# Performance work log

Measured on AMD Instinct MI355X. Metric: run time of the kernel, lower is better.

Reference implementation:

```python
import jax, jax.numpy as jnp
import numpy as np

B, S, D, H = 2, 2048, 1024, 16
HD = D // H  # 64


def setup_inputs() -> dict:
    key = jax.random.key(0)
    k1, k2, k3, k4, k5, k6 = jax.random.split(key, 6)
    x = jax.random.normal(k1, (B, S, D), dtype=jnp.float32)
    # binary mask source (1.0 = masked-out position), multiplied by -1e9 inside
    mask = (jax.random.uniform(k2, (B, S, S), dtype=jnp.float32) < 0.1).astype(jnp.float32)
    lim = 1.0 / np.sqrt(D)
    Wqkv = jax.random.uniform(k3, (D, 3 * D), dtype=jnp.float32, minval=-lim, maxval=lim)
    bqkv = jax.random.uniform(k4, (3 * D,), dtype=jnp.float32, minval=-lim, maxval=lim)
    Wo = jax.random.uniform(k5, (D, D), dtype=jnp.float32, minval=-lim, maxval=lim)
    bo = jax.random.uniform(k6, (D,), dtype=jnp.float32, minval=-lim, maxval=lim)
    return {"x": x, "mask": mask, "Wqkv": Wqkv, "bqkv": bqkv, "Wo": Wo, "bo": bo}


def reference(x, mask, Wqkv, bqkv, Wo, bo):
    b, s, d = x.shape
    qkv = x @ Wqkv + bqkv                              # [B,S,3D]
    qkv = qkv.reshape(b, s, 3, H, HD).transpose(2, 0, 3, 1, 4)  # [3,B,H,S,HD]
    q, k, v = qkv[0], qkv[1], qkv[2]
    scale = 1.0 / jnp.sqrt(jnp.float32(HD))
    scores = jnp.einsum('bhqd,bhkd->bhqk', q, k) * scale
    scores = scores + mask[:, None, :, :] * (-1e9)     # broadcast over heads
    attn = jax.nn.softmax(scores, axis=-1)             # [B,H,S,S]
    values = jnp.einsum('bhqk,bhkd->bhqd', attn, v)    # [B,H,S,HD]
    # faithful to source: permute(1,0,2,3) then reshape(B,S,H*HD)
    values = values.transpose(1, 0, 2, 3).reshape(b, s, H * HD)
    return values @ Wo + bo
```

## Files before the change

### kernel.cpp

```cpp
#include <hip/hip_runtime.h>
#include <stdint.h>

#define BB 2
#define SS 2048
#define DD 1024
#define HH 16
#define HD 64
#define BH 32
#define BS 4096

typedef short bf16x8 __attribute__((ext_vector_type(8)));
typedef float f32x4 __attribute__((ext_vector_type(4)));

static __device__ __forceinline__ unsigned short f2bf(float f) {
    union { float f; unsigned int u; } x;
    x.f = f;
    unsigned int u = x.u;
    unsigned int r = u + 0x7FFFu + ((u >> 16) & 1u);
    return (unsigned short)(r >> 16);
}

static __device__ __forceinline__ void gld16(unsigned short* lds, const unsigned short* g) {
    __builtin_amdgcn_global_load_lds(
        (const __attribute__((address_space(1))) unsigned int*)g,
        (__attribute__((address_space(3))) unsigned int*)lds,
        16, 0, 0);
}

__global__ __launch_bounds__(256) void prep(
    const float* __restrict__ x, unsigned short* __restrict__ xb,
    const float* __restrict__ Wqkv, unsigned short* __restrict__ WqkvT,
    const float* __restrict__ Wo, unsigned short* __restrict__ WoT,
    const float* __restrict__ mask, unsigned int* __restrict__ mbitsT,
    unsigned int* __restrict__ kmaxsq) {
    __shared__ float tile[32][33];
    int bid = blockIdx.x;
    int tid = threadIdx.x;
    if (bid < 4096) {
        int i = (bid * 256 + tid) * 4;
        float4 v = *(const float4*)(x + i);
        ushort4 o;
        o.x = f2bf(v.x); o.y = f2bf(v.y); o.z = f2bf(v.z); o.w = f2bf(v.w);
        *(ushort4*)(xb + i) = o;
    } else if (bid < 8192) {
        const float* W;
        unsigned short* WT;
        int N, t;
        if (bid < 7168) { W = Wqkv; WT = WqkvT; N = 3072; t = bid - 4096; }
        else            { W = Wo;   WT = WoT;   N = 1024; t = bid - 7168; }
        const int K = 1024;
        int nx = N >> 5;
        int n0 = (t % nx) * 32, k0 = (t / nx) * 32;
        int tx = tid & 31, ty = tid >> 5;
#pragma unroll
        for (int i = 0; i < 4; i++)
            tile[ty + i * 8][tx] = W[(size_t)(k0 + ty + i * 8) * N + n0 + tx];
        __syncthreads();
#pragma unroll
        for (int i = 0; i < 4; i++)
            WT[(size_t)(n0 + ty + i * 8) * K + k0 + tx] = f2bf(tile[tx][ty + i * 8]);
    } else if (bid == 8192) {
        if (tid < BH) kmaxsq[tid] = 0u;
    } else {
        size_t i = (size_t)(bid - 8193) * 256 + tid;
        float v = mask[i];
        unsigned long long bal = __ballot(v != 0.0f);
        int lane = tid & 63;
        int kw = (int)((i & 2047) >> 5);
        int sq = (int)((i >> 11) & 2047);
        int b = (int)(i >> 22);
        if (lane == 0)
            mbitsT[((size_t)b * 64 + kw) * 2048 + sq] = (unsigned int)bal;
        else if (lane == 32)
            mbitsT[((size_t)b * 64 + kw) * 2048 + sq] = (unsigned int)(bal >> 32);
    }
}

__global__ __launch_bounds__(256) void k_norm_max(
    const unsigned short* __restrict__ k_ws, unsigned int* __restrict__ kmaxsq) {
    int bh = blockIdx.x >> 3, part = blockIdx.x & 7;
    int row = part * 256 + threadIdx.x;
    const unsigned short* rp = k_ws + ((size_t)bh * 2048 + row) * 64;
    float ss = 0.f;
#pragma unroll
    for (int i = 0; i < 64; i += 8) {
        bf16x8 v;
        __builtin_memcpy(&v, rp + i, 16);
#pragma unroll
        for (int j = 0; j < 8; j++) {
            float f = __uint_as_float(((unsigned int)(unsigned short)v[j]) << 16);
            ss += f * f;
        }
    }
#pragma unroll
    for (int d = 1; d < 64; d <<= 1) ss = fmaxf(ss, __shfl_xor(ss, d, 64));
    if ((threadIdx.x & 63) == 0) atomicMax(kmaxsq + bh, __float_as_uint(ss));
}

__global__ __launch_bounds__(256) void qkv_gemm(
    const unsigned short* __restrict__ xb,
    const unsigned short* __restrict__ WqkvT,
    const float* __restrict__ bqkv,
    unsigned short* __restrict__ q_ws,
    unsigned short* __restrict__ k_ws,
    unsigned short* __restrict__ vB) {
    __shared__ unsigned short ldsA[4096], ldsB[4096];
    int gx = blockIdx.x;
    int tid = threadIdx.x;
    int m0 = (gx / 24) * 128, n0 = (gx % 24) * 128;
    int w = tid >> 6, lane = tid & 63, quad = lane >> 4, l15 = lane & 15;

    int r = tid >> 2, p = tid & 3;
    int c = (p - (r >> 1)) & 3;
    const unsigned short* gA0 = xb + (size_t)(m0 + r) * 1024 + c * 8;
    const unsigned short* gA1 = gA0 + (size_t)64 * 1024;
    const unsigned short* gB0 = WqkvT + (size_t)(n0 + r) * 1024 + c * 8;
    const unsigned short* gB1 = gB0 + (size_t)64 * 1024;
    unsigned short* lA0 = ldsA + w * 512;
    unsigned short* lA1 = ldsA + 2048 + w * 512;
    unsigned short* lB0 = ldsB + w * 512;
    unsigned short* lB1 = ldsB + 2048 + w * 512;

    int wm = w >> 1, wn = w & 1;
    int posq = ((quad + (l15 >> 1)) & 3) * 8;
    int aoff = (wm * 64 + l15) * 32 + posq;
    int boff = (wn * 64 + l15) * 32 + posq;

    f32x4 acc[4][4] = {};
    for (int k0 = 0; k0 < 1024; k0 += 32) {
        __syncthreads();
        gld16(lA0, gA0 + k0);
        gld16(lA1, gA1 + k0);
        gld16(lB0, gB0 + k0);
        gld16(lB1, gB1 + k0);
        __syncthreads();
        bf16x8 af[4], bfr[4];
#pragma unroll
        for (int i = 0; i < 4; i++) {
            af[i]  = *(const bf16x8*)(ldsA + aoff + i * 512);
            bfr[i] = *(const bf16x8*)(ldsB + boff + i * 512);
        }
#pragma unroll
        for (int i = 0; i < 4; i++)
#pragma unroll
            for (int j = 0; j < 4; j++)
                acc[i][j] = __builtin_amdgcn_mfma_f32_16x16x32_bf16(af[i], bfr[j], acc[i][j], 0, 0, 0);
    }

    int t = n0 >> 10;
    int ncol0 = n0 + wn * 64;
    int hh = (ncol0 >> 6) & 15;
    int Rb = m0 + wm * 64 + quad * 4;

    if (t == 2) {
        int rowbase = m0 + wm * 64;
        int b = rowbase >> 11;
        int kt = (rowbase >> 6) & 31;
        int bh = b * 16 + hh;
#pragma unroll
        for (int j = 0; j < 4; j++) {
            int hd = j * 16 + l15;
            float bias = bqkv[ncol0 + hd];
#pragma unroll
            for (int i = 0; i < 4; i++) {
                unsigned short* dst = vB +
                    (((((size_t)bh * 32 + kt) * 2 + (i >> 1)) * 4 + quad) * 64 + hd) * 8 + (i & 1) * 4;
                ushort4 pk;
                pk.x = f2bf(acc[i][j][0] + bias);
                pk.y = f2bf(acc[i][j][1] + bias);
                pk.z = f2bf(acc[i][j][2] + bias);
                pk.w = f2bf(acc[i][j][3] + bias);
                *(ushort4*)dst = pk;
            }
        }
    } else {
        unsigned short* dst = (t == 0) ? q_ws : k_ws;
#pragma unroll
        for (int j = 0; j < 4; j++) {
            int hd = j * 16 + l15;
            float bias = bqkv[ncol0 + hd];
#pragma unroll
            for (int i = 0; i < 4; i++) {
                int row = Rb + i * 16;
                int b = row >> 11, s = row & 2047;
                int bh = b * 16 + hh;
#pragma unroll
                for (int rr = 0; rr < 4; rr++)
                    dst[((size_t)(bh * 2048 + s + rr)) * 64 + hd] = f2bf(acc[i][j][rr] + bias);
            }
        }
    }
}

__global__ __launch_bounds__(256) void out_gemm(
    const unsigned short* __restrict__ Amat,
    const unsigned short* __restrict__ WoT,
    const float* __restrict__ bo,
    float* __restrict__ out) {
    __shared__ unsigned short ldsA[4096], ldsB[2048];
    int gx = blockIdx.x;
    int m0 = (gx / 16) * 128, n0 = (gx % 16) * 64;
    int tid = threadIdx.x;
    int w = tid >> 6, lane = tid & 63, quad = lane >> 4, l15 = lane & 15;

    int r = tid >> 2, p = tid & 3;
    int c = (p - (r >> 1)) & 3;
    const unsigned short* gA0 = Amat + (size_t)(m0 + r) * 1024 + c * 8;
    const unsigned short* gA1 = gA0 + (size_t)64 * 1024;
    const unsigned short* gB0 = WoT + (size_t)(n0 + r) * 1024 + c * 8;
    unsigned short* lA0 = ldsA + w * 512;
    unsigned short* lA1 = ldsA + 2048 + w * 512;
    unsigned short* lB0 = ldsB + w * 512;

    int wm = w >> 1, wn = w & 1;
    int posq = ((quad + (l15 >> 1)) & 3) * 8;
    int aoff = (wm * 64 + l15) * 32 + posq;
    int boff = (wn * 32 + l15) * 32 + posq;

    f32x4 acc[4][2] = {};
    for (int k0 = 0; k0 < 1024; k0 += 32) {
        __syncthreads();
        gld16(lA0, gA0 + k0);
        gld16(lA1, gA1 + k0);
        gld16(lB0, gB0 + k0);
        __syncthreads();
        bf16x8 af[4], bfr[2];
#pragma unroll
        for (int i = 0; i < 4; i++) af[i] = *(const bf16x8*)(ldsA + aoff + i * 512);
#pragma unroll
        for (int j = 0; j < 2; j++) bfr[j] = *(const bf16x8*)(ldsB + boff + j * 512);
#pragma unroll
        for (int i = 0; i < 4; i++)
#pragma unroll
            for (int j = 0; j < 2; j++)
                acc[i][j] = __builtin_amdgcn_mfma_f32_16x16x32_bf16(af[i], bfr[j], acc[i][j], 0, 0, 0);
    }
    int ncol0 = n0 + wn * 32;
    int Rb = m0 + wm * 64 + quad * 4;
#pragma unroll
    for (int j = 0; j < 2; j++) {
        int col = ncol0 + j * 16 + l15;
        float bias = bo[col];
#pragma unroll
        for (int i = 0; i < 4; i++) {
            int row = Rb + i * 16;
#pragma unroll
            for (int rr = 0; rr < 4; rr++)
                out[(size_t)(row + rr) * 1024 + col] = acc[i][j][rr] + bias;
        }
    }
}

__global__ __launch_bounds__(256) void attn(
    const unsigned short* __restrict__ q_ws,
    const unsigned short* __restrict__ k_ws,
    const unsigned short* __restrict__ vB,
    const unsigned int* __restrict__ mbitsT,
    const unsigned int* __restrict__ kmaxsq,
    unsigned short* __restrict__ o_ws) {
    __shared__ float ocomb[2][64][33];
    __shared__ float lcomb[2][32];

    int tid = threadIdx.x;
    int w = tid >> 6, lane = tid & 63, quad = lane >> 4, l15 = lane & 15;
    int wq = w & 1, wk = w >> 1;
    int bx = blockIdx.x;
    int bh = bx >> 5, qt = bx & 31;
    int b = bh >> 4, h = bh & 15;
    int qtb = qt * 64;

    bf16x8 qf[2][2];
#pragma unroll
    for (int nt = 0; nt < 2; nt++) {
        const unsigned short* qp =
            q_ws + ((size_t)(bh * 2048 + qtb + wq * 32 + nt * 16 + l15)) * 64 + quad * 8;
        qf[nt][0] = *(const bf16x8*)(qp);
        qf[nt][1] = *(const bf16x8*)(qp + 32);
    }

    float ssn[2];
#pragma unroll
    for (int nt = 0; nt < 2; nt++) {
        float ss = 0.f;
#pragma unroll
        for (int ks = 0; ks < 2; ks++)
#pragma unroll
            for (int j = 0; j < 8; j++) {
                float a = __uint_as_float(((unsigned int)(unsigned short)qf[nt][ks][j]) << 16);
                ss += a * a;
            }
        ss += __shfl_xor(ss, 16, 64);
        ss += __shfl_xor(ss, 32, 64);
        ssn[nt] = ss;
    }
    const float c2 = 0.125f * 1.44269504089f;
    float Km = sqrtf(__uint_as_float(kmaxsq[bh]));
    const float Cs = c2 * 8388608.0f;
    float Ds[2];
#pragma unroll
    for (int nt = 0; nt < 2; nt++) {
        float M = sqrtf(ssn[nt]) * Km * c2 * 1.01f + 0.05f;
        Ds[nt] = (127.0f - M) * 8388608.0f;
    }

    const unsigned short* kbase = k_ws + (size_t)bh * 2048 * 64
                                  + (size_t)(wk * 32 + l15) * 64 + quad * 8;
    const unsigned short* vbase = vB + (size_t)bh * 32 * 4096
                                  + (size_t)(wk * 4 + quad) * 512 + l15 * 8;
    const unsigned int* mbq = mbitsT + (size_t)b * 64 * 2048 + qtb + wq * 32 + l15;

    f32x4 oacc[4][2] = {};
    f32x4 lacc[2] = {};
    bf16x8 onesA;
#pragma unroll
    for (int j = 0; j < 8; j++) onesA[j] = (short)0x3F80;

    int q4 = quad * 4;

    bf16x8 kf[2][2][2];
    unsigned int mw[2][2];
#pragma unroll
    for (int mg = 0; mg < 2; mg++) {
        kf[0][mg][0] = *(const bf16x8*)(kbase + mg * 1024);
        kf[0][mg][1] = *(const bf16x8*)(kbase + mg * 1024 + 32);
    }
    mw[0][0] = mbq[(size_t)wk * 2048];
    mw[0][1] = mbq[(size_t)wk * 2048 + 16];

#pragma unroll 2
    for (int kt = 0; kt < 32; kt++) {
        int par = kt & 1, nxt = par ^ 1;
        if (kt < 31) {
            const unsigned short* kp = kbase + (size_t)(kt + 1) * 4096;
#pragma unroll
            for (int mg = 0; mg < 2; mg++) {
                kf[nxt][mg][0] = *(const bf16x8*)(kp + mg * 1024);
                kf[nxt][mg][1] = *(const bf16x8*)(kp + mg * 1024 + 32);
            }
            mw[nxt][0] = mbq[(size_t)((kt + 1) * 2 + wk) * 2048];
            mw[nxt][1] = mbq[(size_t)((kt + 1) * 2 + wk) * 2048 + 16];
        }
        bf16x8 vf[4];
        {
            const unsigned short* vp = vbase + (size_t)kt * 4096;
#pragma unroll
            for (int hdg = 0; hdg < 4; hdg++)
                vf[hdg] = *(const bf16x8*)(vp + hdg * 128);
        }
        f32x4 sacc[2][2];
#pragma unroll
        for (int mg = 0; mg < 2; mg++)
#pragma unroll
            for (int nt = 0; nt < 2; nt++) {
                f32x4 z = {};
                z = __builtin_amdgcn_mfma_f32_16x16x32_bf16(kf[par][mg][0], qf[nt][0], z, 0, 0, 0);
                z = __builtin_amdgcn_mfma_f32_16x16x32_bf16(kf[par][mg][1], qf[nt][1], z, 0, 0, 0);
                sacc[mg][nt] = z;
            }
#pragma unroll
        for (int nt = 0; nt < 2; nt++) {
            unsigned int sel = mw[par][nt] >> q4;
            union { bf16x8 v; unsigned int d[4]; } bfr;
#pragma unroll
            for (int mg = 0; mg < 2; mg++) {
                unsigned int u[4];
#pragma unroll
                for (int rr = 0; rr < 4; rr++) {
                    float y = __builtin_fmaf(sacc[mg][nt][rr], Cs, Ds[nt]);
                    if ((sel >> (mg * 16 + rr)) & 1u) y = 0.f;
                    u[rr] = (unsigned int)(int)y;
                }
                bfr.d[mg * 2 + 0] = __builtin_amdgcn_perm(u[1], u[0], 0x07060302u);
                bfr.d[mg * 2 + 1] = __builtin_amdgcn_perm(u[3], u[2], 0x07060302u);
            }
#pragma unroll
            for (int hdg = 0; hdg < 4; hdg++)
                oacc[hdg][nt] = __builtin_amdgcn_mfma_f32_16x16x32_bf16(vf[hdg], bfr.v, oacc[hdg][nt], 0, 0, 0);
            lacc[nt] = __builtin_amdgcn_mfma_f32_16x16x32_bf16(onesA, bfr.v, lacc[nt], 0, 0, 0);
        }
    }

    if (wk == 1) {
#pragma unroll
        for (int hdg = 0; hdg < 4; hdg++)
#pragma unroll
            for (int nt = 0; nt < 2; nt++)
#pragma unroll
                for (int rr = 0; rr < 4; rr++)
                    ocomb[wq][hdg * 16 + quad * 4 + rr][nt * 16 + l15] = oacc[hdg][nt][rr];
        if (quad == 0) {
            lcomb[wq][l15] = lacc[0][0];
            lcomb[wq][16 + l15] = lacc[1][0];
        }
    }
    __syncthreads();
    if (wk == 0) {
        float linv[2];
#pragma unroll
        for (int nt = 0; nt < 2; nt++)
            linv[nt] = 1.0f / (lacc[nt][0] + lcomb[wq][nt * 16 + l15]);
#pragma unroll
        for (int nt = 0; nt < 2; nt++) {
            int q = qtb + wq * 32 + nt * 16 + l15;
            unsigned short* base = o_ws + ((size_t)((h * 2 + b) * 2048 + q)) * 64;
#pragma unroll
            for (int hdg = 0; hdg < 4; hdg++) {
                ushort4 pk;
                pk.x = f2bf((oacc[hdg][nt][0] + ocomb[wq][hdg * 16 + quad * 4 + 0][nt * 16 + l15]) * linv[nt]);
                pk.y = f2bf((oacc[hdg][nt][1] + ocomb[wq][hdg * 16 + quad * 4 + 1][nt * 16 + l15]) * linv[nt]);
                pk.z = f2bf((oacc[hdg][nt][2] + ocomb[wq][hdg * 16 + quad * 4 + 2][nt * 16 + l15]) * linv[nt]);
                pk.w = f2bf((oacc[hdg][nt][3] + ocomb[wq][hdg * 16 + quad * 4 + 3][nt * 16 + l15]) * linv[nt]);
                *(ushort4*)(base + hdg * 16 + quad * 4) = pk;
            }
        }
    }
}


extern "C" void kernel_launch(void* const* d_in, const int* in_sizes, int n_in,
                              void* d_out, int out_size, void* d_ws, size_t ws_size,
                              hipStream_t stream) {
    const float* x    = (const float*)d_in[0];
    const float* mask = (const float*)d_in[1];
    const float* Wqkv = (const float*)d_in[2];
    const float* bqkv = (const float*)d_in[3];
    const float* Wo   = (const float*)d_in[4];
    const float* bo   = (const float*)d_in[5];
    float* out = (float*)d_out;

    char* ws = (char*)d_ws;
    unsigned short* xb    = (unsigned short*)(ws);
    unsigned short* WqkvT = (unsigned short*)(ws + ((size_t)8 << 20));
    unsigned short* WoT   = (unsigned short*)(ws + ((size_t)14 << 20));
    unsigned short* q_ws  = (unsigned short*)(ws + ((size_t)16 << 20));
    unsigned short* k_ws  = (unsigned short*)(ws + ((size_t)24 << 20));
    unsigned short* vB    = (unsigned short*)(ws + ((size_t)32 << 20));
    unsigned short* o_ws  = (unsigned short*)(ws + ((size_t)40 << 20));
    unsigned int*   mbits = (unsigned int*)(ws + ((size_t)48 << 20));
    unsigned int*   kmaxsq = (unsigned int*)(ws + ((size_t)49 << 20));

    prep<<<8193 + 32768, 256, 0, stream>>>(x, xb, Wqkv, WqkvT, Wo, WoT, mask, mbits, kmaxsq);
    qkv_gemm<<<768, 256, 0, stream>>>(xb, WqkvT, bqkv, q_ws, k_ws, vB);
    k_norm_max<<<BH * 8, 256, 0, stream>>>(k_ws, kmaxsq);
    attn<<<1024, 256, 0, stream>>>(q_ws, k_ws, vB, mbits, kmaxsq, o_ws);
    out_gemm<<<512, 256, 0, stream>>>(o_ws, WoT, bo, out);
}
```

Before: 264.2 us.

## Stage K and V tiles through LDS with async global_load_lds and swizzle

```diff
diff --git a/kernel.cpp b/kernel.cpp
--- a/kernel.cpp
+++ b/kernel.cpp
@@ -258,8 +258,10 @@
     const unsigned int* __restrict__ mbitsT,
     const unsigned int* __restrict__ kmaxsq,
     unsigned short* __restrict__ o_ws) {
-    __shared__ float ocomb[2][64][33];
-    __shared__ float lcomb[2][32];
+    __shared__ union ShMem {
+        struct { unsigned short K[4096]; unsigned short V[4096]; } tiles;
+        struct { float ocomb[2][64][33]; float lcomb[2][32]; } comb;
+    } sh;
 
     int tid = threadIdx.x;
     int w = tid >> 6, lane = tid & 63, quad = lane >> 4, l15 = lane & 15;
@@ -278,36 +280,40 @@
         qf[nt][1] = *(const bf16x8*)(qp + 32);
     }
 
-    float ssn[2];
-#pragma unroll
-    for (int nt = 0; nt < 2; nt++) {
-        float ss = 0.f;
-#pragma unroll
-        for (int ks = 0; ks < 2; ks++)
-#pragma unroll
-            for (int j = 0; j < 8; j++) {
-                float a = __uint_as_float(((unsigned int)(unsigned short)qf[nt][ks][j]) << 16);
-                ss += a * a;
-            }
-        ss += __shfl_xor(ss, 16, 64);
-        ss += __shfl_xor(ss, 32, 64);
-        ssn[nt] = ss;
-    }
     const float c2 = 0.125f * 1.44269504089f;
     float Km = sqrtf(__uint_as_float(kmaxsq[bh]));
     const float Cs = c2 * 8388608.0f;
     float Ds[2];
 #pragma unroll
     for (int nt = 0; nt < 2; nt++) {
-        float M = sqrtf(ssn[nt]) * Km * c2 * 1.01f + 0.05f;
+        float ss = 0.f;
+#pragma unroll
+        for (int ks = 0; ks < 2; ks++)
+#pragma unroll
+            for (int j = 0; j < 8; j++) {
+                float a = __uint_as_float(((unsigned int)(unsigned short)qf[nt][ks][j]) << 16);
+                ss += a * a;
+            }
+        ss += __shfl_xor(ss, 16, 64);
+        ss += __shfl_xor(ss, 32, 64);
+        float M = sqrtf(ss) * Km * c2 * 1.01f + 0.05f;
         Ds[nt] = (127.0f - M) * 8388608.0f;
     }
 
-    const unsigned short* kbase = k_ws + (size_t)bh * 2048 * 64
-                                  + (size_t)(wk * 32 + l15) * 64 + quad * 8;
-    const unsigned short* vbase = vB + (size_t)bh * 32 * 4096
-                                  + (size_t)(wk * 4 + quad) * 512 + l15 * 8;
     const unsigned int* mbq = mbitsT + (size_t)b * 64 * 2048 + qtb + wq * 32 + l15;
+    const unsigned short* kbase = k_ws + (size_t)bh * 2048 * 64;
+    const unsigned short* vbb = vB + (size_t)bh * 32 * 4096;
+
+    int srow = lane >> 3;
+    int spos = lane & 7;
+    unsigned short* dK0 = sh.tiles.K + w * 1024 + lane * 8;
+    unsigned short* dK1 = dK0 + 512;
+    unsigned short* dV0 = sh.tiles.V + w * 1024 + lane * 8;
+    unsigned short* dV1 = dV0 + 512;
+    int r0 = w * 16 + srow;
+    int r1 = r0 + 8;
+    int g0 = spos ^ (r0 & 7);
+    int g1 = spos ^ (r1 & 7);
 
     f32x4 oacc[4][2] = {};
     f32x4 lacc[2] = {};
@@ -315,51 +321,46 @@
 #pragma unroll
     for (int j = 0; j < 8; j++) onesA[j] = (short)0x3F80;
 
+    int sw = l15 & 7;
     int q4 = quad * 4;
 
-    bf16x8 kf[2][2][2];
-    unsigned int mw[2][2];
-#pragma unroll
-    for (int mg = 0; mg < 2; mg++) {
-        kf[0][mg][0] = *(const bf16x8*)(kbase + mg * 1024);
-        kf[0][mg][1] = *(const bf16x8*)(kbase + mg * 1024 + 32);
-    }
-    mw[0][0] = mbq[(size_t)wk * 2048];
-    mw[0][1] = mbq[(size_t)wk * 2048 + 16];
-
-#pragma unroll 2
     for (int kt = 0; kt < 32; kt++) {
-        int par = kt & 1, nxt = par ^ 1;
-        if (kt < 31) {
-            const unsigned short* kp = kbase + (size_t)(kt + 1) * 4096;
-#pragma unroll
-            for (int mg = 0; mg < 2; mg++) {
-                kf[nxt][mg][0] = *(const bf16x8*)(kp + mg * 1024);
-                kf[nxt][mg][1] = *(const bf16x8*)(kp + mg * 1024 + 32);
-            }
-            mw[nxt][0] = mbq[(size_t)((kt + 1) * 2 + wk) * 2048];
-            mw[nxt][1] = mbq[(size_t)((kt + 1) * 2 + wk) * 2048 + 16];
-        }
-        bf16x8 vf[4];
+        __syncthreads();
+        gld16(dK0, kbase + ((size_t)(kt * 64 + r0)) * 64 + g0 * 8);
+        gld16(dK1, kbase + ((size_t)(kt * 64 + r1)) * 64 + g1 * 8);
         {
-            const unsigned short* vp = vbase + (size_t)kt * 4096;
-#pragma unroll
-            for (int hdg = 0; hdg < 4; hdg++)
-                vf[hdg] = *(const bf16x8*)(vp + hdg * 128);
-        }
+            const unsigned short* vsrc = vbb + (size_t)kt * 4096 + w * 1024 + lane * 8;
+            gld16(dV0, vsrc);
+            gld16(dV1, vsrc + 512);
+        }
+        unsigned int mwv[2];
+        mwv[0] = mbq[(size_t)(2 * kt + wk) * 2048];
+        mwv[1] = mbq[(size_t)(2 * kt + wk) * 2048 + 16];
+        __syncthreads();
+
         f32x4 sacc[2][2];
 #pragma unroll
-        for (int mg = 0; mg < 2; mg++)
+        for (int mg = 0; mg < 2; mg++) {
+            const unsigned short* kr = sh.tiles.K + (wk * 32 + mg * 16 + l15) * 64;
+            bf16x8 kf0, kf1;
+            __builtin_memcpy(&kf0, kr + (quad ^ sw) * 8, 16);
+            __builtin_memcpy(&kf1, kr + ((quad + 4) ^ sw) * 8, 16);
 #pragma unroll
             for (int nt = 0; nt < 2; nt++) {
                 f32x4 z = {};
-                z = __builtin_amdgcn_mfma_f32_16x16x32_bf16(kf[par][mg][0], qf[nt][0], z, 0, 0, 0);
-                z = __builtin_amdgcn_mfma_f32_16x16x32_bf16(kf[par][mg][1], qf[nt][1], z, 0, 0, 0);
+                z = __builtin_amdgcn_mfma_f32_16x16x32_bf16(kf0, qf[nt][0], z, 0, 0, 0);
+                z = __builtin_amdgcn_mfma_f32_16x16x32_bf16(kf1, qf[nt][1], z, 0, 0, 0);
                 sacc[mg][nt] = z;
             }
+        }
+        bf16x8 vf[4];
+#pragma unroll
+        for (int hdg = 0; hdg < 4; hdg++)
+            __builtin_memcpy(&vf[hdg],
+                             sh.tiles.V + ((wk * 4 + quad) * 64 + hdg * 16 + l15) * 8, 16);
 #pragma unroll
         for (int nt = 0; nt < 2; nt++) {
-            unsigned int sel = mw[par][nt] >> q4;
+            unsigned int sel = mwv[nt] >> q4;
             union { bf16x8 v; unsigned int d[4]; } bfr;
 #pragma unroll
             for (int mg = 0; mg < 2; mg++) {
@@ -380,6 +381,7 @@
         }
     }
 
+    __syncthreads();
     if (wk == 1) {
 #pragma unroll
         for (int hdg = 0; hdg < 4; hdg++)
@@ -387,10 +389,10 @@
             for (int nt = 0; nt < 2; nt++)
 #pragma unroll
                 for (int rr = 0; rr < 4; rr++)
-                    ocomb[wq][hdg * 16 + quad * 4 + rr][nt * 16 + l15] = oacc[hdg][nt][rr];
+                    sh.comb.ocomb[wq][hdg * 16 + q4 + rr][nt * 16 + l15] = oacc[hdg][nt][rr];
         if (quad == 0) {
-            lcomb[wq][l15] = lacc[0][0];
-            lcomb[wq][16 + l15] = lacc[1][0];
+            sh.comb.lcomb[wq][l15] = lacc[0][0];
+            sh.comb.lcomb[wq][16 + l15] = lacc[1][0];
         }
     }
     __syncthreads();
@@ -398,7 +400,7 @@
         float linv[2];
 #pragma unroll
         for (int nt = 0; nt < 2; nt++)
-            linv[nt] = 1.0f / (lacc[nt][0] + lcomb[wq][nt * 16 + l15]);
+            linv[nt] = 1.0f / (lacc[nt][0] + sh.comb.lcomb[wq][nt * 16 + l15]);
 #pragma unroll
         for (int nt = 0; nt < 2; nt++) {
             int q = qtb + wq * 32 + nt * 16 + l15;
@@ -406,11 +408,11 @@
 #pragma unroll
             for (int hdg = 0; hdg < 4; hdg++) {
                 ushort4 pk;
-                pk.x = f2bf((oacc[hdg][nt][0] + ocomb[wq][hdg * 16 + quad * 4 + 0][nt * 16 + l15]) * linv[nt]);
-                pk.y = f2bf((oacc[hdg][nt][1] + ocomb[wq][hdg * 16 + quad * 4 + 1][nt * 16 + l15]) * linv[nt]);
-                pk.z = f2bf((oacc[hdg][nt][2] + ocomb[wq][hdg * 16 + quad * 4 + 2][nt * 16 + l15]) * linv[nt]);
-                pk.w = f2bf((oacc[hdg][nt][3] + ocomb[wq][hdg * 16 + quad * 4 + 3][nt * 16 + l15]) * linv[nt]);
-                *(ushort4*)(base + hdg * 16 + quad * 4) = pk;
+                pk.x = f2bf((oacc[hdg][nt][0] + sh.comb.ocomb[wq][hdg * 16 + q4 + 0][nt * 16 + l15]) * linv[nt]);
+                pk.y = f2bf((oacc[hdg][nt][1] + sh.comb.ocomb[wq][hdg * 16 + q4 + 1][nt * 16 + l15]) * linv[nt]);
+                pk.z = f2bf((oacc[hdg][nt][2] + sh.comb.ocomb[wq][hdg * 16 + q4 + 2][nt * 16 + l15]) * linv[nt]);
+                pk.w = f2bf((oacc[hdg][nt][3] + sh.comb.ocomb[wq][hdg * 16 + q4 + 3][nt * 16 + l15]) * linv[nt]);
+                *(ushort4*)(base + hdg * 16 + q4) = pk;
             }
         }
     }
```

After: 270.3 us. 1.02x slower.
